# Optimization experiments

Hardware: AMD Instinct MI355X
Metric: run time of the kernel (lower is better)

## Reference

```python
import jax, jax.numpy as jnp
import numpy as np

B, MAXN, NVT, NINP, NHID, NHEAD, NL, NZ = 1024, 32, 16, 256, 512, 8, 6, 64
HID = MAXN * NHID
EPS = 1e-5
SCALE = 1.0 / np.sqrt(NHID // NHEAD)


def setup_inputs() -> dict:
    key = jax.random.key(0)
    ks = jax.random.split(key, 16)
    s = 0.02
    d = {}
    d["node_types"] = jax.random.randint(ks[0], (B, MAXN), 0, NVT, dtype=jnp.int32)
    d["adj_bits"] = jax.random.randint(ks[1], (B, MAXN, MAXN), 0, 2, dtype=jnp.int32)
    d["Wpos"] = jax.random.normal(ks[2], (MAXN, NINP), jnp.float32) * s
    d["bpos"] = jnp.zeros((NINP,), jnp.float32)
    d["Wnode"] = jax.random.normal(ks[3], (NVT, NINP), jnp.float32) * s
    d["bnode"] = jnp.zeros((NINP,), jnp.float32)
    for i, n in enumerate(["Wq", "Wk", "Wv", "Wo", "W1", "W2"]):
        d["enc_" + n] = jax.random.normal(ks[4 + i], (NL, NHID, NHID), jnp.float32) * s
    for n in ["bq", "bk", "bv", "bo", "b1", "b2"]:
        d["enc_" + n] = jnp.zeros((NL, NHID), jnp.float32)
    d["ln1_g"] = jnp.ones((NL, NHID), jnp.float32)
    d["ln1_b"] = jnp.zeros((NL, NHID), jnp.float32)
    d["ln2_g"] = jnp.ones((NL, NHID), jnp.float32)
    d["ln2_b"] = jnp.zeros((NL, NHID), jnp.float32)
    d["Wfc1"] = jax.random.normal(ks[10], (HID, NZ), jnp.float32) * s
    d["bfc1"] = jnp.zeros((NZ,), jnp.float32)
    d["Wfc2"] = jax.random.normal(ks[11], (HID, NZ), jnp.float32) * s
    d["bfc2"] = jnp.zeros((NZ,), jnp.float32)
    return d


def _ln(x, g, b):
    m = x.mean(-1, keepdims=True)
    v = ((x - m) ** 2).mean(-1, keepdims=True)
    return (x - m) * jax.lax.rsqrt(v + EPS) * g + b


def _dag_attn_bias(adj_bits):
    # _mask_generate: transitive closure via matmul powers; log-depth squaring
    # over a boolean semiring (min(.,1) after each add) gives identical reachability.
    iu = jnp.triu(jnp.ones((MAXN, MAXN), jnp.float32), 1)  # enforce DAG
    adj = adj_bits.astype(jnp.float32) * iu  # [B,N,N]
    reach = adj
    for _ in range(int(np.ceil(np.log2(MAXN)))):
        reach = jnp.minimum(reach + jnp.matmul(reach, reach), 1.0)
    # original: mask = (sum_powers + I) < 0.5 (True=disallowed), then transpose(1,2)
    allowed = (jnp.swapaxes(reach, 1, 2) + jnp.eye(MAXN, dtype=jnp.float32)) > 0.5
    return jnp.where(allowed, 0.0, -jnp.inf)[:, None, :, :]  # [B,1,N,N]


def _encode(node_types, adj_bits, Wpos, bpos, Wnode, bnode,
            enc_Wq, enc_bq, enc_Wk, enc_bk, enc_Wv, enc_bv, enc_Wo, enc_bo,
            ln1_g, ln1_b, enc_W1, enc_b1, enc_W2, enc_b2, ln2_g, ln2_b,
            Wfc1, bfc1, Wfc2, bfc2):
    node_feat = jax.nn.relu(Wnode[node_types] + bnode)               # [B,N,ninp]
    pos_feat = jnp.broadcast_to(Wpos + bpos, (B, MAXN, NINP))        # position = node index
    x = jnp.concatenate([node_feat, pos_feat], -1)                   # [B,N,512]
    bias = _dag_attn_bias(adj_bits)
    dh = NHID // NHEAD
    for l in range(NL):
        q = (x @ enc_Wq[l] + enc_bq[l]).reshape(B, MAXN, NHEAD, dh)
        k = (x @ enc_Wk[l] + enc_bk[l]).reshape(B, MAXN, NHEAD, dh)
        v = (x @ enc_Wv[l] + enc_bv[l]).reshape(B, MAXN, NHEAD, dh)
        s = jnp.einsum('bqhd,bkhd->bhqk', q, k) * SCALE + bias
        a = jax.nn.softmax(s, axis=-1)
        o = jnp.einsum('bhqk,bkhd->bqhd', a, v).reshape(B, MAXN, NHID)
        x = _ln(x + o @ enc_Wo[l] + enc_bo[l], ln1_g[l], ln1_b[l])    # post-LN
        f = jax.nn.relu(x @ enc_W1[l] + enc_b1[l]) @ enc_W2[l] + enc_b2[l]
        x = _ln(x + f, ln2_g[l], ln2_b[l])
    mem = x.reshape(B, HID)
    return mem @ Wfc1 + bfc1, mem @ Wfc2 + bfc2


def reference(node_types, adj_bits, Wpos, bpos, Wnode, bnode,
              enc_Wq, enc_bq, enc_Wk, enc_bk, enc_Wv, enc_bv, enc_Wo, enc_bo,
              ln1_g, ln1_b, enc_W1, enc_b1, enc_W2, enc_b2, ln2_g, ln2_b,
              Wfc1, bfc1, Wfc2, bfc2):
    return _encode(node_types, adj_bits, Wpos, bpos, Wnode, bnode,
                   enc_Wq, enc_bq, enc_Wk, enc_bk, enc_Wv, enc_bv, enc_Wo, enc_bo,
                   ln1_g, ln1_b, enc_W1, enc_b1, enc_W2, enc_b2, ln2_g, ln2_b,
                   Wfc1, bfc1, Wfc2, bfc2)
```

## Files before the change

### kernel.cpp

```cpp
#include <hip/hip_runtime.h>


typedef unsigned short u16;
typedef unsigned int u32;
typedef __attribute__((ext_vector_type(8))) short bf16x8;
typedef __attribute__((ext_vector_type(4))) float f32x4;

#define NB 1024
#define MAXN 32
#define NHID 512
#define NHEAD 8
#define NLAY 6
#define MTOT (NB * MAXN)
#define ATT_SCALE 0.125f
#define LN_EPS 1e-5f

__device__ __forceinline__ float bf2f(u16 h) { return __uint_as_float(((u32)h) << 16); }
__device__ __forceinline__ u16 f2bf(float f) {
  u32 u = __float_as_uint(f);
  return (u16)((u + 0x7fffu + ((u >> 16) & 1u)) >> 16);
}

__device__ __forceinline__ void gload16(const void* g, void* l) {
  __builtin_amdgcn_global_load_lds((const __attribute__((address_space(1))) void*)g,
                                   (__attribute__((address_space(3))) void*)l, 16, 0, 0);
}

__device__ __forceinline__ void xcd_remap(int l, int NX, int& mt, int& nt) {
  int xcd = l & 7;
  int s = l >> 3;
  int mg = s / NX;
  nt = s - mg * NX;
  mt = mg * 8 + xcd;
}

__global__ __launch_bounds__(256) void mask_k(const int* __restrict__ adj, u32* __restrict__ mask) {
  __shared__ u32 r[8][32];
  int tid = threadIdx.x;
  int g = tid >> 5, i = tid & 31;
  int b = blockIdx.x * 8 + g;
  const int* ab = adj + ((long)b * 32 + i) * 32;
  u32 m = 0;
  for (int j = i + 1; j < 32; ++j)
    if (ab[j]) m |= (1u << j);
  r[g][i] = m;
  __syncthreads();
  for (int it = 0; it < 5; ++it) {
    u32 cur = r[g][i];
    u32 acc = cur;
    #pragma unroll
    for (int j = 0; j < 32; ++j)
      if ((cur >> j) & 1u) acc |= r[g][j];
    __syncthreads();
    r[g][i] = acc;
    __syncthreads();
  }
  u32 am = 1u << i;
  #pragma unroll
  for (int k = 0; k < 32; ++k) am |= ((r[g][k] >> i) & 1u) << k;
  mask[b * 32 + i] = am;
}

__global__ __launch_bounds__(256) void embed_k(const int* __restrict__ types,
    const float* __restrict__ Wpos, const float* __restrict__ bpos,
    const float* __restrict__ Wnode, const float* __restrict__ bnode,
    u16* __restrict__ xb) {
  int i = blockIdx.x * 256 + threadIdx.x;
  int row = i >> 7, c = (i & 127) * 4;
  int b = row >> 5, n = row & 31;
  float v[4];
  if (c < 256) {
    int tp = types[b * 32 + n];
    const float* w = &Wnode[tp * 256 + c];
    #pragma unroll
    for (int j = 0; j < 4; ++j) v[j] = fmaxf(w[j] + bnode[c + j], 0.f);
  } else {
    int cc = c - 256;
    const float* w = &Wpos[n * 256 + cc];
    #pragma unroll
    for (int j = 0; j < 4; ++j) v[j] = w[j] + bpos[cc + j];
  }
  ushort4 h; h.x = f2bf(v[0]); h.y = f2bf(v[1]); h.z = f2bf(v[2]); h.w = f2bf(v[3]);
  *(ushort4*)&xb[(long)row * NHID + c] = h;
}

__global__ __launch_bounds__(256) void tconv_k(const float* __restrict__ W,
    u16* __restrict__ Wt, int n_off, int n_total) {
  __shared__ float tile[32][33];
  int l = blockIdx.z;
  int k0 = blockIdx.x * 32, n0 = blockIdx.y * 32;
  int tx = threadIdx.x & 31, ty = threadIdx.x >> 5;
  const float* src = W + (size_t)l * NHID * NHID;
  #pragma unroll
  for (int i = 0; i < 4; ++i)
    tile[ty + 8 * i][tx] = src[(size_t)(k0 + ty + 8 * i) * NHID + n0 + tx];
  __syncthreads();
  u16* dst = Wt + (size_t)l * n_total * NHID;
  #pragma unroll
  for (int i = 0; i < 4; ++i)
    dst[(size_t)(n_off + n0 + ty + 8 * i) * NHID + k0 + tx] = f2bf(tile[tx][ty + 8 * i]);
}

template <int EPI>
__global__ __launch_bounds__(256, 2) void gemm_bt(
    const u16* __restrict__ A, const u16* __restrict__ Bt,
    const float* __restrict__ bias0, const u16* __restrict__ res,
    u16* __restrict__ Cout, int N, int K) {
  __shared__ u16 As[3][128 * 32];
  __shared__ u16 Bs[3][128 * 32];
  const int tid = threadIdx.x;
  const int wave = tid >> 6, lane = tid & 63;
  int mt, nt_;
  xcd_remap(blockIdx.x + gridDim.x * blockIdx.y, gridDim.x, mt, nt_);
  const long m0 = (long)mt * 128;
  const int n0 = nt_ * 128;
  const int wr = wave >> 1, wc = wave & 1;
  const int srow = lane >> 2;
  const int sg = (lane & 3) ^ ((srow >> 1) & 3);
  const int fr = lane & 15;
  const int kq = lane >> 4;
  f32x4 acc[4][4] = {};

  auto stage = [&](int buf, int k0) {
    #pragma unroll
    for (int i = 0; i < 2; ++i) {
      int c = 2 * wave + i;
      gload16(A + (m0 + 16 * c + srow) * (long)K + k0 + sg * 8, &As[buf][c * 512]);
      gload16(Bt + (long)(n0 + 16 * c + srow) * K + k0 + sg * 8, &Bs[buf][c * 512]);
    }
  };
  stage(0, 0);
  stage(1, 32);
  const int nt = K >> 5;
  const int kqx = (kq ^ ((fr >> 1) & 3)) * 8;
  int cs = 0;
  #pragma unroll 1
  for (int t = 0; t < nt; ++t) {
    if (t + 1 < nt) asm volatile("s_waitcnt vmcnt(4)" ::: "memory");
    else            asm volatile("s_waitcnt vmcnt(0)" ::: "memory");
    __builtin_amdgcn_s_barrier();
    if (t + 2 < nt) {
      int nb = cs + 2; if (nb >= 3) nb -= 3;
      stage(nb, (t + 2) * 32);
    }
    const u16* Asl = As[cs];
    const u16* Bsl = Bs[cs];
    bf16x8 af[4], bfv[4];
    #pragma unroll
    for (int mi = 0; mi < 4; ++mi)
      af[mi] = *(const bf16x8*)&Asl[(wr * 64 + mi * 16 + fr) * 32 + kqx];
    #pragma unroll
    for (int ni = 0; ni < 4; ++ni)
      bfv[ni] = *(const bf16x8*)&Bsl[(wc * 64 + ni * 16 + fr) * 32 + kqx];
    #pragma unroll
    for (int mi = 0; mi < 4; ++mi)
      #pragma unroll
      for (int ni = 0; ni < 4; ++ni)
        acc[mi][ni] = __builtin_amdgcn_mfma_f32_16x16x32_bf16(bfv[ni], af[mi], acc[mi][ni], 0, 0, 0);
    if (++cs == 3) cs = 0;
  }

  #pragma unroll
  for (int mi = 0; mi < 4; ++mi) {
    long r = m0 + wr * 64 + mi * 16 + fr;
    #pragma unroll
    for (int ni = 0; ni < 4; ++ni) {
      int n = n0 + wc * 64 + ni * 16 + kq * 4;
      float4 bv = *(const float4*)&bias0[n];
      float v0 = acc[mi][ni][0] + bv.x;
      float v1 = acc[mi][ni][1] + bv.y;
      float v2 = acc[mi][ni][2] + bv.z;
      float v3 = acc[mi][ni][3] + bv.w;
      if (EPI == 2) {
        v0 = fmaxf(v0, 0.f); v1 = fmaxf(v1, 0.f);
        v2 = fmaxf(v2, 0.f); v3 = fmaxf(v3, 0.f);
      }
      if (EPI == 3) {
        ushort4 rv = *(const ushort4*)&res[r * (long)N + n];
        v0 += bf2f(rv.x); v1 += bf2f(rv.y); v2 += bf2f(rv.z); v3 += bf2f(rv.w);
      }
      ushort4 st;
      st.x = f2bf(v0); st.y = f2bf(v1); st.z = f2bf(v2); st.w = f2bf(v3);
      *(ushort4*)&Cout[r * (long)N + n] = st;
    }
  }
}

__global__ __launch_bounds__(256, 2) void gemm_qkv(
    const u16* __restrict__ A, const u16* __restrict__ Bt,
    const float* __restrict__ bq, const float* __restrict__ bk,
    const float* __restrict__ bv, u16* __restrict__ qk, u16* __restrict__ v) {
  __shared__ u16 As[3][128 * 32];
  __shared__ u16 Bs[3][128 * 32];
  const int tid = threadIdx.x;
  const int wave = tid >> 6, lane = tid & 63;
  int mt, nt_;
  xcd_remap(blockIdx.x + gridDim.x * blockIdx.y, gridDim.x, mt, nt_);
  const long m0 = (long)mt * 128;
  const int n0 = nt_ * 128;
  const int wr = wave >> 1, wc = wave & 1;
  const int srow = lane >> 2;
  const int sg = (lane & 3) ^ ((srow >> 1) & 3);
  const int fr = lane & 15;
  const int kq = lane >> 4;
  f32x4 acc[4][4] = {};

  auto stage = [&](int buf, int k0) {
    #pragma unroll
    for (int i = 0; i < 2; ++i) {
      int c = 2 * wave + i;
      gload16(A + (m0 + 16 * c + srow) * 512L + k0 + sg * 8, &As[buf][c * 512]);
      gload16(Bt + (long)(n0 + 16 * c + srow) * 512 + k0 + sg * 8, &Bs[buf][c * 512]);
    }
  };
  stage(0, 0);
  stage(1, 32);
  const int kqx = (kq ^ ((fr >> 1) & 3)) * 8;
  int cs = 0;
  #pragma unroll 1
  for (int t = 0; t < 16; ++t) {
    if (t + 1 < 16) asm volatile("s_waitcnt vmcnt(4)" ::: "memory");
    else            asm volatile("s_waitcnt vmcnt(0)" ::: "memory");
    __builtin_amdgcn_s_barrier();
    if (t + 2 < 16) {
      int nb = cs + 2; if (nb >= 3) nb -= 3;
      stage(nb, (t + 2) * 32);
    }
    const u16* Asl = As[cs];
    const u16* Bsl = Bs[cs];
    bf16x8 af[4], bfv[4];
    #pragma unroll
    for (int mi = 0; mi < 4; ++mi)
      af[mi] = *(const bf16x8*)&Asl[(wr * 64 + mi * 16 + fr) * 32 + kqx];
    #pragma unroll
    for (int ni = 0; ni < 4; ++ni)
      bfv[ni] = *(const bf16x8*)&Bsl[(wc * 64 + ni * 16 + fr) * 32 + kqx];
    #pragma unroll
    for (int mi = 0; mi < 4; ++mi)
      #pragma unroll
      for (int ni = 0; ni < 4; ++ni)
        acc[mi][ni] = __builtin_amdgcn_mfma_f32_16x16x32_bf16(bfv[ni], af[mi], acc[mi][ni], 0, 0, 0);
    if (++cs == 3) cs = 0;
  }

  #pragma unroll
  for (int mi = 0; mi < 4; ++mi) {
    long r = m0 + wr * 64 + mi * 16 + fr;
    #pragma unroll
    for (int ni = 0; ni < 4; ++ni) {
      int n = n0 + wc * 64 + ni * 16 + kq * 4;
      const float* bp = (n < 512) ? bq : ((n < 1024) ? bk : bv);
      float4 bvv = *(const float4*)&bp[n & 511];
      ushort4 st;
      st.x = f2bf(acc[mi][ni][0] + bvv.x);
      st.y = f2bf(acc[mi][ni][1] + bvv.y);
      st.z = f2bf(acc[mi][ni][2] + bvv.z);
      st.w = f2bf(acc[mi][ni][3] + bvv.w);
      if (n < 1024) *(ushort4*)&qk[r * 1024 + n] = st;
      else          *(ushort4*)&v[r * 512 + (n - 1024)] = st;
    }
  }
}

__global__ __launch_bounds__(256) void attn_k(const u16* __restrict__ qk,
    const u16* __restrict__ vfull, const u32* __restrict__ mask, u16* __restrict__ o) {
  __shared__ u16 vs_[4][64][40];
  __shared__ u16 p_lds[4][32][40];
  int tid = threadIdx.x;
  int w = tid >> 6, lane = tid & 63;
  int idx = blockIdx.x * 4 + w;
  int b = idx >> 3, h = idx & 7;
  const u16* qbase = qk + (long)b * 32 * 1024 + h * 64;
  const u16* kbase = qbase + 512;
  int g = lane >> 4, r = lane & 15;

  int node = lane >> 1, dh = lane & 1;
  const u16* vsrc = vfull + ((long)b * 32 + node) * 512 + h * 64 + dh * 32;
  bf16x8 vr[4];
  #pragma unroll
  for (int i = 0; i < 4; ++i) vr[i] = *(const bf16x8*)(vsrc + i * 8);

  f32x4 s[2][2] = {};
  #pragma unroll
  for (int ks = 0; ks < 2; ++ks) {
    bf16x8 kf[2], qf[2];
    #pragma unroll
    for (int mi = 0; mi < 2; ++mi)
      kf[mi] = *(const bf16x8*)(kbase + (long)(mi * 16 + r) * 1024 + ks * 32 + g * 8);
    #pragma unroll
    for (int nj = 0; nj < 2; ++nj)
      qf[nj] = *(const bf16x8*)(qbase + (long)(nj * 16 + r) * 1024 + ks * 32 + g * 8);
    #pragma unroll
    for (int mi = 0; mi < 2; ++mi)
      #pragma unroll
      for (int nj = 0; nj < 2; ++nj)
        s[mi][nj] = __builtin_amdgcn_mfma_f32_16x16x32_bf16(kf[mi], qf[nj], s[mi][nj], 0, 0, 0);
  }

  #pragma unroll
  for (int i = 0; i < 4; ++i)
    #pragma unroll
    for (int t = 0; t < 8; ++t)
      vs_[w][dh * 32 + i * 8 + t][node] = (u16)vr[i][t];

  #pragma unroll
  for (int nj = 0; nj < 2; ++nj) {
    int q = nj * 16 + r;
    u32 mk = mask[b * 32 + q];
    float vv[8];
    float mx = -1e30f;
    #pragma unroll
    for (int mi = 0; mi < 2; ++mi)
      #pragma unroll
      for (int j = 0; j < 4; ++j) {
        int k = mi * 16 + g * 4 + j;
        float val = ((mk >> k) & 1u) ? s[mi][nj][j] * ATT_SCALE : -1e30f;
        vv[mi * 4 + j] = val;
        mx = fmaxf(mx, val);
      }
    mx = fmaxf(mx, __shfl_xor(mx, 16));
    mx = fmaxf(mx, __shfl_xor(mx, 32));
    float sum = 0.f;
    #pragma unroll
    for (int i = 0; i < 8; ++i) { vv[i] = __expf(vv[i] - mx); sum += vv[i]; }
    sum += __shfl_xor(sum, 16);
    sum += __shfl_xor(sum, 32);
    float inv = 1.f / sum;
    #pragma unroll
    for (int mi = 0; mi < 2; ++mi) {
      ushort4 pk;
      pk.x = f2bf(vv[mi * 4 + 0] * inv);
      pk.y = f2bf(vv[mi * 4 + 1] * inv);
      pk.z = f2bf(vv[mi * 4 + 2] * inv);
      pk.w = f2bf(vv[mi * 4 + 3] * inv);
      *(ushort4*)&p_lds[w][q][mi * 16 + g * 4] = pk;
    }
  }

  bf16x8 pa[2];
  #pragma unroll
  for (int mi = 0; mi < 2; ++mi)
    pa[mi] = *(const bf16x8*)&p_lds[w][mi * 16 + r][g * 8];
  f32x4 oacc[2][4] = {};
  #pragma unroll
  for (int nd = 0; nd < 4; ++nd) {
    bf16x8 vf = *(const bf16x8*)&vs_[w][nd * 16 + r][g * 8];
    #pragma unroll
    for (int mi = 0; mi < 2; ++mi)
      oacc[mi][nd] = __builtin_amdgcn_mfma_f32_16x16x32_bf16(pa[mi], vf, oacc[mi][nd], 0, 0, 0);
  }
  #pragma unroll
  for (int mi = 0; mi < 2; ++mi)
    #pragma unroll
    for (int j = 0; j < 4; ++j) {
      int q = mi * 16 + g * 4 + j;
      u16* og = o + ((long)b * 32 + q) * NHID + h * 64;
      #pragma unroll
      for (int nd = 0; nd < 4; ++nd)
        og[nd * 16 + r] = f2bf(oacc[mi][nd][j]);
    }
}

__global__ __launch_bounds__(256) void ln_k(const u16* __restrict__ y,
    const float* __restrict__ g, const float* __restrict__ b, u16* __restrict__ xb) {
  int tid = threadIdx.x;
  int w = tid >> 6, lane = tid & 63;
  long row = (long)blockIdx.x * 4 + w;
  int c = lane * 8;
  long o = row * NHID + c;
  ushort4 a0 = *(const ushort4*)&y[o];
  ushort4 a1 = *(const ushort4*)&y[o + 4];
  float v[8] = {bf2f(a0.x), bf2f(a0.y), bf2f(a0.z), bf2f(a0.w),
                bf2f(a1.x), bf2f(a1.y), bf2f(a1.z), bf2f(a1.w)};
  float s = 0.f, sq = 0.f;
  #pragma unroll
  for (int j = 0; j < 8; ++j) { s += v[j]; sq += v[j] * v[j]; }
  #pragma unroll
  for (int off = 1; off < 64; off <<= 1) {
    s += __shfl_xor(s, off);
    sq += __shfl_xor(sq, off);
  }
  float mean = s * (1.f / 512.f);
  float inv = rsqrtf(sq * (1.f / 512.f) - mean * mean + LN_EPS);
  float4 ga = *(const float4*)&g[c], gb = *(const float4*)&g[c + 4];
  float4 ba = *(const float4*)&b[c], bb = *(const float4*)&b[c + 4];
  float gg[8] = {ga.x, ga.y, ga.z, ga.w, gb.x, gb.y, gb.z, gb.w};
  float bv[8] = {ba.x, ba.y, ba.z, ba.w, bb.x, bb.y, bb.z, bb.w};
  ushort4 o0, o1;
  o0.x = f2bf((v[0] - mean) * inv * gg[0] + bv[0]);
  o0.y = f2bf((v[1] - mean) * inv * gg[1] + bv[1]);
  o0.z = f2bf((v[2] - mean) * inv * gg[2] + bv[2]);
  o0.w = f2bf((v[3] - mean) * inv * gg[3] + bv[3]);
  o1.x = f2bf((v[4] - mean) * inv * gg[4] + bv[4]);
  o1.y = f2bf((v[5] - mean) * inv * gg[5] + bv[5]);
  o1.z = f2bf((v[6] - mean) * inv * gg[6] + bv[6]);
  o1.w = f2bf((v[7] - mean) * inv * gg[7] + bv[7]);
  *(ushort4*)&xb[o] = o0;
  *(ushort4*)&xb[o + 4] = o1;
}

__global__ __launch_bounds__(256) void fcT_k(const float* __restrict__ W1,
    const float* __restrict__ W2, u16* __restrict__ Wt) {
  __shared__ float t[64][65];
  int sel = blockIdx.y;
  const float* W = sel ? W2 : W1;
  int k0 = blockIdx.x * 64;
  int tx = threadIdx.x & 63, ty = threadIdx.x >> 6;
  #pragma unroll
  for (int i = 0; i < 16; ++i)
    t[ty + 4 * i][tx] = W[(long)(k0 + ty + 4 * i) * 64 + tx];
  __syncthreads();
  #pragma unroll
  for (int i = 0; i < 16; ++i)
    Wt[(long)(sel * 64 + ty + 4 * i) * 16384 + k0 + tx] = f2bf(t[tx][ty + 4 * i]);
}

__global__ __launch_bounds__(256, 2) void gemm_fc(const u16* __restrict__ A,
    const u16* __restrict__ Bt, float* __restrict__ part) {
  __shared__ u16 As[3][128 * 32];
  __shared__ u16 Bs[3][128 * 32];
  const int tid = threadIdx.x;
  const int wave = tid >> 6, lane = tid & 63;
  const int ks = blockIdx.x;
  const long m0 = (long)blockIdx.y * 128;
  const int kbase = ks * 512;
  const int wr = wave >> 1, wc = wave & 1;
  const int srow = lane >> 2;
  const int sg = (lane & 3) ^ ((srow >> 1) & 3);
  const int fr = lane & 15;
  const int kq = lane >> 4;
  f32x4 acc[4][4] = {};
  auto stage = [&](int buf, int k0) {
    #pragma unroll
    for (int i = 0; i < 2; ++i) {
      int c = 2 * wave + i;
      gload16(A + (m0 + 16 * c + srow) * 16384L + kbase + k0 + sg * 8, &As[buf][c * 512]);
      gload16(Bt + (long)(16 * c + srow) * 16384L + kbase + k0 + sg * 8, &Bs[buf][c * 512]);
    }
  };
  stage(0, 0);
  stage(1, 32);
  const int kqx = (kq ^ ((fr >> 1) & 3)) * 8;
  int cs = 0;
  #pragma unroll 1
  for (int t = 0; t < 16; ++t) {
    if (t + 1 < 16) asm volatile("s_waitcnt vmcnt(4)" ::: "memory");
    else            asm volatile("s_waitcnt vmcnt(0)" ::: "memory");
    __builtin_amdgcn_s_barrier();
    if (t + 2 < 16) {
      int nb = cs + 2; if (nb >= 3) nb -= 3;
      stage(nb, (t + 2) * 32);
    }
    const u16* Asl = As[cs];
    const u16* Bsl = Bs[cs];
    bf16x8 af[4], bfv[4];
    #pragma unroll
    for (int mi = 0; mi < 4; ++mi)
      af[mi] = *(const bf16x8*)&Asl[(wr * 64 + mi * 16 + fr) * 32 + kqx];
    #pragma unroll
    for (int ni = 0; ni < 4; ++ni)
      bfv[ni] = *(const bf16x8*)&Bsl[(wc * 64 + ni * 16 + fr) * 32 + kqx];
    #pragma unroll
    for (int mi = 0; mi < 4; ++mi)
      #pragma unroll
      for (int ni = 0; ni < 4; ++ni)
        acc[mi][ni] = __builtin_amdgcn_mfma_f32_16x16x32_bf16(bfv[ni], af[mi], acc[mi][ni], 0, 0, 0);
    if (++cs == 3) cs = 0;
  }
  #pragma unroll
  for (int mi = 0; mi < 4; ++mi) {
    long rr = m0 + wr * 64 + mi * 16 + fr;
    #pragma unroll
    for (int ni = 0; ni < 4; ++ni) {
      int n = wc * 64 + ni * 16 + kq * 4;
      *(float4*)&part[((long)ks * 1024 + rr) * 128 + n] =
          make_float4(acc[mi][ni][0], acc[mi][ni][1], acc[mi][ni][2], acc[mi][ni][3]);
    }
  }
}

__global__ __launch_bounds__(256) void fc_red_k(const float* __restrict__ part,
    const float* __restrict__ bfc1, const float* __restrict__ bfc2,
    float* __restrict__ out) {
  int idx = blockIdx.x * 256 + threadIdx.x;
  int sel = idx >> 16;
  int rem = idx & 65535;
  int b = rem >> 6, z = rem & 63;
  float v = sel ? bfc2[z] : bfc1[z];
  #pragma unroll
  for (int ks = 0; ks < 32; ++ks)
    v += part[((long)ks * 1024 + b) * 128 + sel * 64 + z];
  out[idx] = v;
}

extern "C" void kernel_launch(void* const* d_in, const int* in_sizes, int n_in,
                              void* d_out, int out_size, void* d_ws, size_t ws_size,
                              hipStream_t stream) {
  const int* node_types = (const int*)d_in[0];
  const int* adj_bits = (const int*)d_in[1];
  const float* Wpos = (const float*)d_in[2];
  const float* bpos = (const float*)d_in[3];
  const float* Wnode = (const float*)d_in[4];
  const float* bnode = (const float*)d_in[5];
  const float* eWq = (const float*)d_in[6];
  const float* eWk = (const float*)d_in[7];
  const float* eWv = (const float*)d_in[8];
  const float* eWo = (const float*)d_in[9];
  const float* eW1 = (const float*)d_in[10];
  const float* eW2 = (const float*)d_in[11];
  const float* ebq = (const float*)d_in[12];
  const float* ebk = (const float*)d_in[13];
  const float* ebv = (const float*)d_in[14];
  const float* ebo = (const float*)d_in[15];
  const float* eb1 = (const float*)d_in[16];
  const float* eb2 = (const float*)d_in[17];
  const float* ln1g = (const float*)d_in[18];
  const float* ln1b = (const float*)d_in[19];
  const float* ln2g = (const float*)d_in[20];
  const float* ln2b = (const float*)d_in[21];
  const float* Wfc1 = (const float*)d_in[22];
  const float* bfc1 = (const float*)d_in[23];
  const float* Wfc2 = (const float*)d_in[24];
  const float* bfc2 = (const float*)d_in[25];

  char* ws = (char*)d_ws;
  size_t off = 0;
  auto carve = [&](size_t bytes) {
    void* p = ws + off;
    off += (bytes + 255) & ~(size_t)255;
    return p;
  };
  u16* Wqkv_t = (u16*)carve((size_t)NLAY * 1536 * 512 * 2);
  u16* Wo_t = (u16*)carve((size_t)NLAY * 512 * 512 * 2);
  u16* W1_t = (u16*)carve((size_t)NLAY * 512 * 512 * 2);
  u16* W2_t = (u16*)carve((size_t)NLAY * 512 * 512 * 2);
  u16* xb = (u16*)carve((size_t)MTOT * NHID * 2);
  u16* qk = (u16*)carve((size_t)MTOT * 1024 * 2);
  u16* vbuf = (u16*)carve((size_t)MTOT * NHID * 2);
  u16* obuf = (u16*)carve((size_t)MTOT * NHID * 2);
  u32* maskb = (u32*)carve((size_t)NB * MAXN * 4);
  u16* ybuf = qk;
  u16* hbuf = obuf;
  u16* Wt_fc = qk;
  float* part_fc = (float*)obuf;

  mask_k<<<NB / 8, 256, 0, stream>>>(adj_bits, maskb);
  embed_k<<<(MTOT * 128) / 256, 256, 0, stream>>>(node_types, Wpos, bpos, Wnode, bnode, xb);
  dim3 tg(16, 16, NLAY);
  tconv_k<<<tg, 256, 0, stream>>>(eWq, Wqkv_t, 0, 1536);
  tconv_k<<<tg, 256, 0, stream>>>(eWk, Wqkv_t, 512, 1536);
  tconv_k<<<tg, 256, 0, stream>>>(eWv, Wqkv_t, 1024, 1536);
  tconv_k<<<tg, 256, 0, stream>>>(eWo, Wo_t, 0, 512);
  tconv_k<<<tg, 256, 0, stream>>>(eW1, W1_t, 0, 512);
  tconv_k<<<tg, 256, 0, stream>>>(eW2, W2_t, 0, 512);

  for (int l = 0; l < NLAY; ++l) {
    size_t lw = (size_t)l * 512 * 512;
    gemm_qkv<<<dim3(12, MTOT / 128), 256, 0, stream>>>(
        xb, Wqkv_t + (size_t)l * 1536 * 512,
        ebq + l * 512, ebk + l * 512, ebv + l * 512, qk, vbuf);
    attn_k<<<NB * NHEAD / 4, 256, 0, stream>>>(qk, vbuf, maskb, obuf);
    gemm_bt<3><<<dim3(4, MTOT / 128), 256, 0, stream>>>(
        obuf, Wo_t + lw, ebo + l * 512, xb, ybuf, 512, 512);
    ln_k<<<MTOT / 4, 256, 0, stream>>>(ybuf, ln1g + l * 512, ln1b + l * 512, xb);
    gemm_bt<2><<<dim3(4, MTOT / 128), 256, 0, stream>>>(
        xb, W1_t + lw, eb1 + l * 512, nullptr, hbuf, 512, 512);
    gemm_bt<3><<<dim3(4, MTOT / 128), 256, 0, stream>>>(
        hbuf, W2_t + lw, eb2 + l * 512, xb, ybuf, 512, 512);
    ln_k<<<MTOT / 4, 256, 0, stream>>>(ybuf, ln2g + l * 512, ln2b + l * 512, xb);
  }

  fcT_k<<<dim3(256, 2), 256, 0, stream>>>(Wfc1, Wfc2, Wt_fc);
  gemm_fc<<<dim3(32, 8), 256, 0, stream>>>(xb, Wt_fc, part_fc);
  fc_red_k<<<512, 256, 0, stream>>>(part_fc, bfc1, bfc2, (float*)d_out);
}
```

Measured before the change: 1.429 ms.

## Fuse residual and LayerNorm into full-row GEMMs and widen N tiles

Replaces the generic gemm_bt plus separate ln_k passes with gemm_ln. This 512-thread kernel computes a full 512-wide output row block, adds bias and residual, and does the LayerNorm reduction in registers and LDS before writing xb in place. This removes the intermediate ybuf write and re-read and two kernel launches per layer. It also widens the QKV and FFN1 GEMM N-tile from 128 to 256 to cut A-tile reloads. The cost is larger LDS use (about 120 KB), more accumulator registers, one block per CU, and a grid of only 256 blocks for the LN GEMMs.

Measured after the change: 1.361 ms. -4.8%, faster.

```diff
diff --git a/kernel.cpp b/kernel.cpp
--- a/kernel.cpp
+++ b/kernel.cpp
@@ -101,115 +101,34 @@
     dst[(size_t)(n_off + n0 + ty + 8 * i) * NHID + k0 + tx] = f2bf(tile[tx][ty + 8 * i]);
 }
 
-template <int EPI>
-__global__ __launch_bounds__(256, 2) void gemm_bt(
+__global__ __launch_bounds__(256, 2) void gemm_qkv(
     const u16* __restrict__ A, const u16* __restrict__ Bt,
-    const float* __restrict__ bias0, const u16* __restrict__ res,
-    u16* __restrict__ Cout, int N, int K) {
+    const float* __restrict__ bq, const float* __restrict__ bk,
+    const float* __restrict__ bv, u16* __restrict__ qk, u16* __restrict__ v) {
   __shared__ u16 As[3][128 * 32];
-  __shared__ u16 Bs[3][128 * 32];
+  __shared__ u16 Bs[3][256 * 32];
   const int tid = threadIdx.x;
   const int wave = tid >> 6, lane = tid & 63;
   int mt, nt_;
   xcd_remap(blockIdx.x + gridDim.x * blockIdx.y, gridDim.x, mt, nt_);
   const long m0 = (long)mt * 128;
-  const int n0 = nt_ * 128;
+  const int n0 = nt_ * 256;
   const int wr = wave >> 1, wc = wave & 1;
   const int srow = lane >> 2;
   const int sg = (lane & 3) ^ ((srow >> 1) & 3);
   const int fr = lane & 15;
   const int kq = lane >> 4;
-  f32x4 acc[4][4] = {};
-
-  auto stage = [&](int buf, int k0) {
-    #pragma unroll
-    for (int i = 0; i < 2; ++i) {
-      int c = 2 * wave + i;
-      gload16(A + (m0 + 16 * c + srow) * (long)K + k0 + sg * 8, &As[buf][c * 512]);
-      gload16(Bt + (long)(n0 + 16 * c + srow) * K + k0 + sg * 8, &Bs[buf][c * 512]);
-    }
-  };
-  stage(0, 0);
-  stage(1, 32);
-  const int nt = K >> 5;
-  const int kqx = (kq ^ ((fr >> 1) & 3)) * 8;
-  int cs = 0;
-  #pragma unroll 1
-  for (int t = 0; t < nt; ++t) {
-    if (t + 1 < nt) asm volatile("s_waitcnt vmcnt(4)" ::: "memory");
-    else            asm volatile("s_waitcnt vmcnt(0)" ::: "memory");
-    __builtin_amdgcn_s_barrier();
-    if (t + 2 < nt) {
-      int nb = cs + 2; if (nb >= 3) nb -= 3;
-      stage(nb, (t + 2) * 32);
-    }
-    const u16* Asl = As[cs];
-    const u16* Bsl = Bs[cs];
-    bf16x8 af[4], bfv[4];
-    #pragma unroll
-    for (int mi = 0; mi < 4; ++mi)
-      af[mi] = *(const bf16x8*)&Asl[(wr * 64 + mi * 16 + fr) * 32 + kqx];
-    #pragma unroll
-    for (int ni = 0; ni < 4; ++ni)
-      bfv[ni] = *(const bf16x8*)&Bsl[(wc * 64 + ni * 16 + fr) * 32 + kqx];
-    #pragma unroll
-    for (int mi = 0; mi < 4; ++mi)
-      #pragma unroll
-      for (int ni = 0; ni < 4; ++ni)
-        acc[mi][ni] = __builtin_amdgcn_mfma_f32_16x16x32_bf16(bfv[ni], af[mi], acc[mi][ni], 0, 0, 0);
-    if (++cs == 3) cs = 0;
-  }
-
-  #pragma unroll
-  for (int mi = 0; mi < 4; ++mi) {
-    long r = m0 + wr * 64 + mi * 16 + fr;
-    #pragma unroll
-    for (int ni = 0; ni < 4; ++ni) {
-      int n = n0 + wc * 64 + ni * 16 + kq * 4;
-      float4 bv = *(const float4*)&bias0[n];
-      float v0 = acc[mi][ni][0] + bv.x;
-      float v1 = acc[mi][ni][1] + bv.y;
-      float v2 = acc[mi][ni][2] + bv.z;
-      float v3 = acc[mi][ni][3] + bv.w;
-      if (EPI == 2) {
-        v0 = fmaxf(v0, 0.f); v1 = fmaxf(v1, 0.f);
-        v2 = fmaxf(v2, 0.f); v3 = fmaxf(v3, 0.f);
-      }
-      if (EPI == 3) {
-        ushort4 rv = *(const ushort4*)&res[r * (long)N + n];
-        v0 += bf2f(rv.x); v1 += bf2f(rv.y); v2 += bf2f(rv.z); v3 += bf2f(rv.w);
-      }
-      ushort4 st;
-      st.x = f2bf(v0); st.y = f2bf(v1); st.z = f2bf(v2); st.w = f2bf(v3);
-      *(ushort4*)&Cout[r * (long)N + n] = st;
-    }
-  }
-}
-
-__global__ __launch_bounds__(256, 2) void gemm_qkv(
-    const u16* __restrict__ A, const u16* __restrict__ Bt,
-    const float* __restrict__ bq, const float* __restrict__ bk,
-    const float* __restrict__ bv, u16* __restrict__ qk, u16* __restrict__ v) {
-  __shared__ u16 As[3][128 * 32];
-  __shared__ u16 Bs[3][128 * 32];
-  const int tid = threadIdx.x;
-  const int wave = tid >> 6, lane = tid & 63;
-  int mt, nt_;
-  xcd_remap(blockIdx.x + gridDim.x * blockIdx.y, gridDim.x, mt, nt_);
-  const long m0 = (long)mt * 128;
-  const int n0 = nt_ * 128;
-  const int wr = wave >> 1, wc = wave & 1;
-  const int srow = lane >> 2;
-  const int sg = (lane & 3) ^ ((srow >> 1) & 3);
-  const int fr = lane & 15;
-  const int kq = lane >> 4;
-  f32x4 acc[4][4] = {};
+  f32x4 acc[4][8] = {};
 
   auto stage = [&](int buf, int k0) {
     #pragma unroll
     for (int i = 0; i < 2; ++i) {
       int c = 2 * wave + i;
       gload16(A + (m0 + 16 * c + srow) * 512L + k0 + sg * 8, &As[buf][c * 512]);
+    }
+    #pragma unroll
+    for (int i = 0; i < 4; ++i) {
+      int c = 4 * wave + i;
       gload16(Bt + (long)(n0 + 16 * c + srow) * 512 + k0 + sg * 8, &Bs[buf][c * 512]);
     }
   };
@@ -219,7 +138,7 @@
   int cs = 0;
   #pragma unroll 1
   for (int t = 0; t < 16; ++t) {
-    if (t + 1 < 16) asm volatile("s_waitcnt vmcnt(4)" ::: "memory");
+    if (t + 1 < 16) asm volatile("s_waitcnt vmcnt(6)" ::: "memory");
     else            asm volatile("s_waitcnt vmcnt(0)" ::: "memory");
     __builtin_amdgcn_s_barrier();
     if (t + 2 < 16) {
@@ -228,17 +147,17 @@
     }
     const u16* Asl = As[cs];
     const u16* Bsl = Bs[cs];
-    bf16x8 af[4], bfv[4];
+    bf16x8 af[4], bfv[8];
     #pragma unroll
     for (int mi = 0; mi < 4; ++mi)
       af[mi] = *(const bf16x8*)&Asl[(wr * 64 + mi * 16 + fr) * 32 + kqx];
     #pragma unroll
-    for (int ni = 0; ni < 4; ++ni)
-      bfv[ni] = *(const bf16x8*)&Bsl[(wc * 64 + ni * 16 + fr) * 32 + kqx];
+    for (int ni = 0; ni < 8; ++ni)
+      bfv[ni] = *(const bf16x8*)&Bsl[(wc * 128 + ni * 16 + fr) * 32 + kqx];
     #pragma unroll
     for (int mi = 0; mi < 4; ++mi)
       #pragma unroll
-      for (int ni = 0; ni < 4; ++ni)
+      for (int ni = 0; ni < 8; ++ni)
         acc[mi][ni] = __builtin_amdgcn_mfma_f32_16x16x32_bf16(bfv[ni], af[mi], acc[mi][ni], 0, 0, 0);
     if (++cs == 3) cs = 0;
   }
@@ -247,8 +166,8 @@
   for (int mi = 0; mi < 4; ++mi) {
     long r = m0 + wr * 64 + mi * 16 + fr;
     #pragma unroll
-    for (int ni = 0; ni < 4; ++ni) {
-      int n = n0 + wc * 64 + ni * 16 + kq * 4;
+    for (int ni = 0; ni < 8; ++ni) {
+      int n = n0 + wc * 128 + ni * 16 + kq * 4;
       const float* bp = (n < 512) ? bq : ((n < 1024) ? bk : bv);
       float4 bvv = *(const float4*)&bp[n & 511];
       ushort4 st;
@@ -258,6 +177,195 @@
       st.w = f2bf(acc[mi][ni][3] + bvv.w);
       if (n < 1024) *(ushort4*)&qk[r * 1024 + n] = st;
       else          *(ushort4*)&v[r * 512 + (n - 1024)] = st;
+    }
+  }
+}
+
+__global__ __launch_bounds__(256, 2) void gemm_relu(
+    const u16* __restrict__ A, const u16* __restrict__ Bt,
+    const float* __restrict__ bias0, u16* __restrict__ Cout) {
+  __shared__ u16 As[3][128 * 32];
+  __shared__ u16 Bs[3][256 * 32];
+  const int tid = threadIdx.x;
+  const int wave = tid >> 6, lane = tid & 63;
+  int mt, nt_;
+  xcd_remap(blockIdx.x + gridDim.x * blockIdx.y, gridDim.x, mt, nt_);
+  const long m0 = (long)mt * 128;
+  const int n0 = nt_ * 256;
+  const int wr = wave >> 1, wc = wave & 1;
+  const int srow = lane >> 2;
+  const int sg = (lane & 3) ^ ((srow >> 1) & 3);
+  const int fr = lane & 15;
+  const int kq = lane >> 4;
+  f32x4 acc[4][8] = {};
+
+  auto stage = [&](int buf, int k0) {
+    #pragma unroll
+    for (int i = 0; i < 2; ++i) {
+      int c = 2 * wave + i;
+      gload16(A + (m0 + 16 * c + srow) * 512L + k0 + sg * 8, &As[buf][c * 512]);
+    }
+    #pragma unroll
+    for (int i = 0; i < 4; ++i) {
+      int c = 4 * wave + i;
+      gload16(Bt + (long)(n0 + 16 * c + srow) * 512 + k0 + sg * 8, &Bs[buf][c * 512]);
+    }
+  };
+  stage(0, 0);
+  stage(1, 32);
+  const int kqx = (kq ^ ((fr >> 1) & 3)) * 8;
+  int cs = 0;
+  #pragma unroll 1
+  for (int t = 0; t < 16; ++t) {
+    if (t + 1 < 16) asm volatile("s_waitcnt vmcnt(6)" ::: "memory");
+    else            asm volatile("s_waitcnt vmcnt(0)" ::: "memory");
+    __builtin_amdgcn_s_barrier();
+    if (t + 2 < 16) {
+      int nb = cs + 2; if (nb >= 3) nb -= 3;
+      stage(nb, (t + 2) * 32);
+    }
+    const u16* Asl = As[cs];
+    const u16* Bsl = Bs[cs];
+    bf16x8 af[4], bfv[8];
+    #pragma unroll
+    for (int mi = 0; mi < 4; ++mi)
+      af[mi] = *(const bf16x8*)&Asl[(wr * 64 + mi * 16 + fr) * 32 + kqx];
+    #pragma unroll
+    for (int ni = 0; ni < 8; ++ni)
+      bfv[ni] = *(const bf16x8*)&Bsl[(wc * 128 + ni * 16 + fr) * 32 + kqx];
+    #pragma unroll
+    for (int mi = 0; mi < 4; ++mi)
+      #pragma unroll
+      for (int ni = 0; ni < 8; ++ni)
+        acc[mi][ni] = __builtin_amdgcn_mfma_f32_16x16x32_bf16(bfv[ni], af[mi], acc[mi][ni], 0, 0, 0);
+    if (++cs == 3) cs = 0;
+  }
+
+  #pragma unroll
+  for (int mi = 0; mi < 4; ++mi) {
+    long r = m0 + wr * 64 + mi * 16 + fr;
+    #pragma unroll
+    for (int ni = 0; ni < 8; ++ni) {
+      int n = n0 + wc * 128 + ni * 16 + kq * 4;
+      float4 bvv = *(const float4*)&bias0[n];
+      ushort4 st;
+      st.x = f2bf(fmaxf(acc[mi][ni][0] + bvv.x, 0.f));
+      st.y = f2bf(fmaxf(acc[mi][ni][1] + bvv.y, 0.f));
+      st.z = f2bf(fmaxf(acc[mi][ni][2] + bvv.z, 0.f));
+      st.w = f2bf(fmaxf(acc[mi][ni][3] + bvv.w, 0.f));
+      *(ushort4*)&Cout[r * 512 + n] = st;
+    }
+  }
+}
+
+__global__ __launch_bounds__(512, 1) void gemm_ln(
+    const u16* __restrict__ A, const u16* __restrict__ Bt,
+    const float* __restrict__ bias0, const float* __restrict__ g,
+    const float* __restrict__ b, u16* __restrict__ xb) {
+  __shared__ u16 As[3][128 * 32];
+  __shared__ u16 Bs[3][512 * 32];
+  __shared__ float red[2][64][4][2];
+  const int tid = threadIdx.x;
+  const int wave = tid >> 6, lane = tid & 63;
+  const long m0 = (long)blockIdx.x * 128;
+  const int wr = wave >> 2, wc = wave & 3;
+  const int srow = lane >> 2;
+  const int sg = (lane & 3) ^ ((srow >> 1) & 3);
+  const int fr = lane & 15;
+  const int kq = lane >> 4;
+  f32x4 acc[4][8] = {};
+
+  auto stage = [&](int buf, int k0) {
+    gload16(A + (m0 + 16 * wave + srow) * 512L + k0 + sg * 8, &As[buf][wave * 512]);
+    #pragma unroll
+    for (int i = 0; i < 4; ++i) {
+      int c = 4 * wave + i;
+      gload16(Bt + (long)(16 * c + srow) * 512 + k0 + sg * 8, &Bs[buf][c * 512]);
+    }
+  };
+  stage(0, 0);
+  stage(1, 32);
+  const int kqx = (kq ^ ((fr >> 1) & 3)) * 8;
+  int cs = 0;
+  #pragma unroll 1
+  for (int t = 0; t < 16; ++t) {
+    if (t + 1 < 16) asm volatile("s_waitcnt vmcnt(5)" ::: "memory");
+    else            asm volatile("s_waitcnt vmcnt(0)" ::: "memory");
+    __builtin_amdgcn_s_barrier();
+    if (t + 2 < 16) {
+      int nb = cs + 2; if (nb >= 3) nb -= 3;
+      stage(nb, (t + 2) * 32);
+    }
+    const u16* Asl = As[cs];
+    const u16* Bsl = Bs[cs];
+    bf16x8 af[4], bfv[8];
+    #pragma unroll
+    for (int mi = 0; mi < 4; ++mi)
+      af[mi] = *(const bf16x8*)&Asl[(wr * 64 + mi * 16 + fr) * 32 + kqx];
+    #pragma unroll
+    for (int ni = 0; ni < 8; ++ni)
+      bfv[ni] = *(const bf16x8*)&Bsl[(wc * 128 + ni * 16 + fr) * 32 + kqx];
+    #pragma unroll
+    for (int mi = 0; mi < 4; ++mi)
+      #pragma unroll
+      for (int ni = 0; ni < 8; ++ni)
+        acc[mi][ni] = __builtin_amdgcn_mfma_f32_16x16x32_bf16(bfv[ni], af[mi], acc[mi][ni], 0, 0, 0);
+    if (++cs == 3) cs = 0;
+  }
+
+  float s[4], sq[4];
+  #pragma unroll
+  for (int mi = 0; mi < 4; ++mi) {
+    long r = m0 + wr * 64 + mi * 16 + fr;
+    float ss = 0.f, qq = 0.f;
+    #pragma unroll
+    for (int ni = 0; ni < 8; ++ni) {
+      int n = wc * 128 + ni * 16 + kq * 4;
+      float4 bvv = *(const float4*)&bias0[n];
+      ushort4 rv = *(const ushort4*)&xb[r * 512 + n];
+      float y0 = acc[mi][ni][0] + bvv.x + bf2f(rv.x);
+      float y1 = acc[mi][ni][1] + bvv.y + bf2f(rv.y);
+      float y2 = acc[mi][ni][2] + bvv.z + bf2f(rv.z);
+      float y3 = acc[mi][ni][3] + bvv.w + bf2f(rv.w);
+      acc[mi][ni][0] = y0; acc[mi][ni][1] = y1;
+      acc[mi][ni][2] = y2; acc[mi][ni][3] = y3;
+      ss += y0 + y1 + y2 + y3;
+      qq += y0 * y0 + y1 * y1 + y2 * y2 + y3 * y3;
+    }
+    s[mi] = ss; sq[mi] = qq;
+  }
+  #pragma unroll
+  for (int mi = 0; mi < 4; ++mi) {
+    s[mi] += __shfl_xor(s[mi], 16);  sq[mi] += __shfl_xor(sq[mi], 16);
+    s[mi] += __shfl_xor(s[mi], 32);  sq[mi] += __shfl_xor(sq[mi], 32);
+  }
+  if (lane < 16) {
+    #pragma unroll
+    for (int mi = 0; mi < 4; ++mi) {
+      red[wr][mi * 16 + fr][wc][0] = s[mi];
+      red[wr][mi * 16 + fr][wc][1] = sq[mi];
+    }
+  }
+  __syncthreads();
+  #pragma unroll
+  for (int mi = 0; mi < 4; ++mi) {
+    int rl = mi * 16 + fr;
+    float S = red[wr][rl][0][0] + red[wr][rl][1][0] + red[wr][rl][2][0] + red[wr][rl][3][0];
+    float Q = red[wr][rl][0][1] + red[wr][rl][1][1] + red[wr][rl][2][1] + red[wr][rl][3][1];
+    float mean = S * (1.f / 512.f);
+    float inv = rsqrtf(Q * (1.f / 512.f) - mean * mean + LN_EPS);
+    long r = m0 + wr * 64 + rl;
+    #pragma unroll
+    for (int ni = 0; ni < 8; ++ni) {
+      int n = wc * 128 + ni * 16 + kq * 4;
+      float4 g4 = *(const float4*)&g[n];
+      float4 b4 = *(const float4*)&b[n];
+      ushort4 st;
+      st.x = f2bf((acc[mi][ni][0] - mean) * inv * g4.x + b4.x);
+      st.y = f2bf((acc[mi][ni][1] - mean) * inv * g4.y + b4.y);
+      st.z = f2bf((acc[mi][ni][2] - mean) * inv * g4.z + b4.z);
+      st.w = f2bf((acc[mi][ni][3] - mean) * inv * g4.w + b4.w);
+      *(ushort4*)&xb[r * 512 + n] = st;
     }
   }
 }
@@ -359,44 +467,6 @@
       for (int nd = 0; nd < 4; ++nd)
         og[nd * 16 + r] = f2bf(oacc[mi][nd][j]);
     }
-}
-
-__global__ __launch_bounds__(256) void ln_k(const u16* __restrict__ y,
-    const float* __restrict__ g, const float* __restrict__ b, u16* __restrict__ xb) {
-  int tid = threadIdx.x;
-  int w = tid >> 6, lane = tid & 63;
-  long row = (long)blockIdx.x * 4 + w;
-  int c = lane * 8;
-  long o = row * NHID + c;
-  ushort4 a0 = *(const ushort4*)&y[o];
-  ushort4 a1 = *(const ushort4*)&y[o + 4];
-  float v[8] = {bf2f(a0.x), bf2f(a0.y), bf2f(a0.z), bf2f(a0.w),
-                bf2f(a1.x), bf2f(a1.y), bf2f(a1.z), bf2f(a1.w)};
-  float s = 0.f, sq = 0.f;
-  #pragma unroll
-  for (int j = 0; j < 8; ++j) { s += v[j]; sq += v[j] * v[j]; }
-  #pragma unroll
-  for (int off = 1; off < 64; off <<= 1) {
-    s += __shfl_xor(s, off);
-    sq += __shfl_xor(sq, off);
-  }
-  float mean = s * (1.f / 512.f);
-  float inv = rsqrtf(sq * (1.f / 512.f) - mean * mean + LN_EPS);
-  float4 ga = *(const float4*)&g[c], gb = *(const float4*)&g[c + 4];
-  float4 ba = *(const float4*)&b[c], bb = *(const float4*)&b[c + 4];
-  float gg[8] = {ga.x, ga.y, ga.z, ga.w, gb.x, gb.y, gb.z, gb.w};
-  float bv[8] = {ba.x, ba.y, ba.z, ba.w, bb.x, bb.y, bb.z, bb.w};
-  ushort4 o0, o1;
-  o0.x = f2bf((v[0] - mean) * inv * gg[0] + bv[0]);
-  o0.y = f2bf((v[1] - mean) * inv * gg[1] + bv[1]);
-  o0.z = f2bf((v[2] - mean) * inv * gg[2] + bv[2]);
-  o0.w = f2bf((v[3] - mean) * inv * gg[3] + bv[3]);
-  o1.x = f2bf((v[4] - mean) * inv * gg[4] + bv[4]);
-  o1.y = f2bf((v[5] - mean) * inv * gg[5] + bv[5]);
-  o1.z = f2bf((v[6] - mean) * inv * gg[6] + bv[6]);
-  o1.w = f2bf((v[7] - mean) * inv * gg[7] + bv[7]);
-  *(ushort4*)&xb[o] = o0;
-  *(ushort4*)&xb[o + 4] = o1;
 }
 
 __global__ __launch_bounds__(256) void fcT_k(const float* __restrict__ W1,
@@ -539,7 +609,6 @@
   u16* vbuf = (u16*)carve((size_t)MTOT * NHID * 2);
   u16* obuf = (u16*)carve((size_t)MTOT * NHID * 2);
   u32* maskb = (u32*)carve((size_t)NB * MAXN * 4);
-  u16* ybuf = qk;
   u16* hbuf = obuf;
   u16* Wt_fc = qk;
   float* part_fc = (float*)obuf;
@@ -556,18 +625,16 @@
 
   for (int l = 0; l < NLAY; ++l) {
     size_t lw = (size_t)l * 512 * 512;
-    gemm_qkv<<<dim3(12, MTOT / 128), 256, 0, stream>>>(
+    gemm_qkv<<<dim3(6, MTOT / 128), 256, 0, stream>>>(
         xb, Wqkv_t + (size_t)l * 1536 * 512,
         ebq + l * 512, ebk + l * 512, ebv + l * 512, qk, vbuf);
     attn_k<<<NB * NHEAD / 4, 256, 0, stream>>>(qk, vbuf, maskb, obuf);
-    gemm_bt<3><<<dim3(4, MTOT / 128), 256, 0, stream>>>(
-        obuf, Wo_t + lw, ebo + l * 512, xb, ybuf, 512, 512);
-    ln_k<<<MTOT / 4, 256, 0, stream>>>(ybuf, ln1g + l * 512, ln1b + l * 512, xb);
-    gemm_bt<2><<<dim3(4, MTOT / 128), 256, 0, stream>>>(
-        xb, W1_t + lw, eb1 + l * 512, nullptr, hbuf, 512, 512);
-    gemm_bt<3><<<dim3(4, MTOT / 128), 256, 0, stream>>>(
-        hbuf, W2_t + lw, eb2 + l * 512, xb, ybuf, 512, 512);
-    ln_k<<<MTOT / 4, 256, 0, stream>>>(ybuf, ln2g + l * 512, ln2b + l * 512, xb);
+    gemm_ln<<<MTOT / 128, 512, 0, stream>>>(
+        obuf, Wo_t + lw, ebo + l * 512, ln1g + l * 512, ln1b + l * 512, xb);
+    gemm_relu<<<dim3(2, MTOT / 128), 256, 0, stream>>>(
+        xb, W1_t + lw, eb1 + l * 512, hbuf);
+    gemm_ln<<<MTOT / 128, 512, 0, stream>>>(
+        hbuf, W2_t + lw, eb2 + l * 512, ln2g + l * 512, ln2b + l * 512, xb);
   }
 
   fcT_k<<<dim3(256, 2), 256, 0, stream>>>(Wfc1, Wfc2, Wt_fc);
```
